# Optimization experiments

Measured on AMD Instinct MI355X. Metric: run time of the kernel, lower is better.

The kernel has to match this reference:

```python
import jax, jax.numpy as jnp
import numpy as np

EPS = 1e-5

def inorm(x):
    # instance norm over time (last) axis; torch.std is unbiased (ddof=1)
    m = jnp.mean(x, axis=-1, keepdims=True)
    s = jnp.sqrt(jnp.var(x, axis=-1, ddof=1, keepdims=True))
    return (x - m) / (s + EPS)

def tinorm(x):
    # time-wise instance norm: normalize over channel axis (dim=1)
    m = jnp.mean(x, axis=1, keepdims=True)
    s = jnp.sqrt(jnp.var(x, axis=1, ddof=1, keepdims=True))
    return (x - m) / (s + EPS)

def adaptive_norm(src, trg, wq, wk, wv, norm_fn):
    # src, trg: [B,C,T]; wq/wk/wv: [out,in] as in nn.Linear
    temp = src.shape[1] ** 0.5
    q = jnp.einsum('bct,oc->bto', norm_fn(src), wq)        # [B,Ts,C]
    k = jnp.einsum('bct,oc->bto', norm_fn(trg), wk)        # [B,Tt,C]
    v = jnp.einsum('bct,oc->bto', trg, wv)                 # [B,Tt,C]
    attn = jax.nn.softmax(jnp.einsum('bsc,btc->bst', q / temp, k), axis=-1)
    mean = jnp.einsum('bst,btc->bsc', attn, v)             # attn-weighted mean
    var = jax.nn.relu(jnp.einsum('bst,btc->bsc', attn, v * v) - mean * mean)
    mean_c = jnp.mean(mean, axis=1)[:, :, None]            # [B,C,1]
    std_c = jnp.sqrt(jnp.mean(var, axis=1))[:, :, None]    # [B,C,1]
    return std_c * inorm(src) + mean_c

def sap(x, w, b):
    # self-attention pooling over axis 1; x: [B,N,C], w: [C], b: [1]
    a = jax.nn.softmax(jnp.einsum('bnc,c->bn', x, w) + b, axis=-1)
    return jnp.einsum('bnc,bn->bc', x, a)

def setup_inputs():
    key = jax.random.key(0)
    ks = jax.random.split(key, 24)
    B, C, Ts, Tt, S = 4, 512, 2048, 2048, 2048
    sc = 1.0 / np.sqrt(C).astype(np.float32)
    return {
        'src': jax.random.normal(ks[0], (B, C, Ts), jnp.float32),
        'trg': jax.random.normal(ks[1], (B, C, Tt), jnp.float32),
        'means': jax.random.normal(ks[2], (B, S, C), jnp.float32),
        'stds': jax.random.uniform(ks[3], (B, S, C), jnp.float32),
        'wq_t': jax.random.normal(ks[4], (C, C), jnp.float32) * sc,
        'wk_t': jax.random.normal(ks[5], (C, C), jnp.float32) * sc,
        'wv_t': jax.random.normal(ks[6], (C, C), jnp.float32) * sc,
        'wq_c': jax.random.normal(ks[7], (C, C), jnp.float32) * sc,
        'wk_c': jax.random.normal(ks[8], (C, C), jnp.float32) * sc,
        'wv_c': jax.random.normal(ks[9], (C, C), jnp.float32) * sc,
        'conv1_w': jax.random.normal(ks[10], (C, 2 * C), jnp.float32) * sc,
        'conv1_b': jax.random.normal(ks[11], (C,), jnp.float32) * 0.02,
        'conv2_w': jax.random.normal(ks[12], (C, C, 3), jnp.float32) * sc,
        'bn_g': jax.random.uniform(ks[13], (C,), jnp.float32, 0.5, 1.5),
        'bn_b': jax.random.normal(ks[14], (C,), jnp.float32) * 0.05,
        'bn_m': jax.random.normal(ks[15], (C,), jnp.float32) * 0.1,
        'bn_v': jax.random.uniform(ks[16], (C,), jnp.float32, 0.5, 1.5),
        'msap_w': jax.random.normal(ks[17], (C,), jnp.float32) * sc,
        'msap_b': jax.random.normal(ks[18], (1,), jnp.float32) * 0.02,
        'ssap_w': jax.random.normal(ks[19], (C,), jnp.float32) * sc,
        'ssap_b': jax.random.normal(ks[20], (1,), jnp.float32) * 0.02,
    }

def reference(src, trg, means, stds, wq_t, wk_t, wv_t, wq_c, wk_c, wv_c,
              conv1_w, conv1_b, conv2_w, bn_g, bn_b, bn_m, bn_v,
              msap_w, msap_b, ssap_w, ssap_b):
    src1 = adaptive_norm(src, trg, wq_t, wk_t, wv_t, tinorm)   # TAN
    src2 = adaptive_norm(src, trg, wq_c, wk_c, wv_c, inorm)    # CAN
    x = jnp.concatenate([src1, src2], axis=1)                  # [B,2C,T]
    # conv1: kernel_size=1 -> pointwise GEMM
    x = jnp.einsum('bct,oc->bot', x, conv1_w) + conv1_b[None, :, None]
    # conv2: Conv1d(k=3, pad=1, bias=False) + BatchNorm1d(eval) + ReLU
    x = jax.lax.conv_general_dilated(x, conv2_w, (1,), 'SAME',
                                     dimension_numbers=('NCH', 'OIH', 'NCH'))
    x = (x - bn_m[None, :, None]) * jax.lax.rsqrt(bn_v[None, :, None] + EPS)
    x = x * bn_g[None, :, None] + bn_b[None, :, None]
    x = jax.nn.relu(x)
    # GLAN
    mean = sap(means, msap_w, msap_b)[:, :, None]              # [B,C,1]
    std = sap(stds, ssap_w, ssap_b)[:, :, None]                # [B,C,1]
    return inorm(x) * std + mean
```

## Files before the change

### kernel.cpp

```cpp
#include <hip/hip_runtime.h>
#include <cstdint>
#include <cstddef>

#define B_ 4
#define C_ 512
#define T_ 2048
#define S_ 2048
#define EPSF 1e-5f

typedef __bf16 bf16;
typedef __attribute__((ext_vector_type(8))) __bf16 bf16x8;
typedef __attribute__((ext_vector_type(4))) float f32x4;

__device__ __forceinline__ bf16 f2b(float f){ return (bf16)f; }
__device__ __forceinline__ float b2f(bf16 h){ return (float)h; }

__device__ __forceinline__ void gl_lds16(const void* g, void* l){
  __builtin_amdgcn_global_load_lds((__attribute__((address_space(1))) void*)(g),
                                   (__attribute__((address_space(3))) void*)(l), 16, 0, 0);
}

__device__ __forceinline__ float wave_sum(float v){
#pragma unroll
  for (int o = 32; o; o >>= 1) v += __shfl_xor(v, o, 64);
  return v;
}
__device__ __forceinline__ float wave_max(float v){
#pragma unroll
  for (int o = 32; o; o >>= 1) v = fmaxf(v, __shfl_xor(v, o, 64));
  return v;
}

template<int EPI, int TNW>
__global__ void __launch_bounds__(256) gemm_nt(
    const bf16* __restrict__ A, const bf16* __restrict__ Bm, void* __restrict__ Cout,
    int K, int lda, int ldb, int ldc,
    long long sA, long long sB, long long sC, long long sCb,
    int zdivA, int zmodB, float scale,
    const float* __restrict__ rs, const float* __restrict__ rsh,
    const float* __restrict__ cbias,
    float* __restrict__ osum, float* __restrict__ osum2, long long sRs,
    float* __restrict__ ocol)
{
  constexpr int TN = TNW*32;
  __shared__ alignas(16) bf16 lA[128*64];
  __shared__ alignas(16) bf16 lB[TN*64];
  __shared__ float redcs[EPI == 3 ? 32*68 : 1];
  const int tid = threadIdx.x;
  const int z = blockIdx.z;
  const bf16* Ab = A + (long long)(z / zdivA) * sA;
  const bf16* Bb = Bm + (long long)(z % zmodB) * sB;
  const int m0 = blockIdx.y*128, n0 = blockIdx.x*TN;
  const int lane = tid & 63, wvi = tid >> 6;
  const int wm = wvi >> 1, wn = wvi & 1;

  f32x4 acc[4][TNW] = {};

  const int lrow = tid >> 3;
  const int lcol = ((tid ^ lrow) & 7) * 8;
  const bf16* pa = Ab + (long long)(m0 + lrow)*lda + lcol;
  const bf16* pb = Bb + (long long)(n0 + lrow)*ldb + lcol;
  char* sa = (char*)lA + tid*16;
  char* sb = (char*)lB + tid*16;

  const int csg = tid >> 3, csph = tid & 7;
  float linv4[4];
  if (EPI == 3) {
#pragma unroll
    for (int rr = 0; rr < 4; ++rr)
      linv4[rr] = 1.f / rs[(long long)z*sRs + (m0 + csg*4 + rr)];
  }

  for (int k0 = 0; k0 < K; k0 += 64) {
#pragma unroll
    for (int it = 0; it < 4; ++it)
      gl_lds16(pa + (long long)it*32*lda + k0, sa + it*4096);
#pragma unroll
    for (int it = 0; it < TNW; ++it)
      gl_lds16(pb + (long long)it*32*ldb + k0, sb + it*4096);
    __syncthreads();
#pragma unroll
    for (int ks = 0; ks < 2; ++ks) {
      const int kq = ks*4 + (lane >> 4);
      bf16x8 af[4], bfr[TNW];
#pragma unroll
      for (int mt = 0; mt < 4; ++mt) {
        int r = wm*64 + mt*16 + (lane & 15);
        af[mt] = *(const bf16x8*)&lA[r*64 + ((kq ^ (r & 7))*8)];
      }
#pragma unroll
      for (int nt = 0; nt < TNW; ++nt) {
        int r = wn*(TNW*16) + nt*16 + (lane & 15);
        bfr[nt] = *(const bf16x8*)&lB[r*64 + ((kq ^ (r & 7))*8)];
      }
#pragma unroll
      for (int mt = 0; mt < 4; ++mt)
#pragma unroll
        for (int nt = 0; nt < TNW; ++nt)
          acc[mt][nt] = __builtin_amdgcn_mfma_f32_16x16x32_bf16(af[mt], bfr[nt], acc[mt][nt], 0, 0, 0);
    }
    bool own = false;
    if (EPI == 3) {
      own = ((k0 >> 6) & 3) == (int)blockIdx.x;
      if (own) {
        float part[8] = {0.f,0.f,0.f,0.f,0.f,0.f,0.f,0.f};
#pragma unroll
        for (int rr = 0; rr < 4; ++rr) {
          const int r = csg*4 + rr;
          bf16x8 v = *(const bf16x8*)&lA[r*64 + ((csph ^ (r & 7))*8)];
          const float li = linv4[rr];
#pragma unroll
          for (int j = 0; j < 8; ++j) part[j] += b2f(v[j]) * li;
        }
#pragma unroll
        for (int j = 0; j < 8; ++j) redcs[csg*68 + csph*8 + j] = part[j];
      }
    }
    __syncthreads();
    if (EPI == 3) {
      if (own && tid < 64) {
        float s = 0.f;
#pragma unroll
        for (int g2 = 0; g2 < 32; ++g2) s += redcs[g2*68 + tid];
        atomicAdd(&ocol[(long long)z*lda + k0 + tid], s);
      }
    }
  }

  if (EPI == 3) {
    float* red1 = (float*)lA;
    float* red2 = red1 + 4*TNW*16;
    const int cr = (lane >> 4)*4;
    float linv[4][4];
#pragma unroll
    for (int mt = 0; mt < 4; ++mt)
#pragma unroll
      for (int i = 0; i < 4; ++i)
        linv[mt][i] = 1.f / rs[(long long)z*sRs + (m0 + wm*64 + mt*16 + cr + i)];
    float s1[TNW], s2[TNW];
#pragma unroll
    for (int nt = 0; nt < TNW; ++nt) {
      s1[nt] = 0.f; s2[nt] = 0.f;
#pragma unroll
      for (int mt = 0; mt < 4; ++mt)
#pragma unroll
        for (int i = 0; i < 4; ++i) {
          float v = acc[mt][nt][i] * linv[mt][i];
          s1[nt] += v; s2[nt] += v*v;
        }
      s1[nt] += __shfl_xor(s1[nt], 16, 64);
      s1[nt] += __shfl_xor(s1[nt], 32, 64);
      s2[nt] += __shfl_xor(s2[nt], 16, 64);
      s2[nt] += __shfl_xor(s2[nt], 32, 64);
    }
    __syncthreads();
    if (lane < 16) {
#pragma unroll
      for (int nt = 0; nt < TNW; ++nt) {
        red1[(wvi*TNW + nt)*16 + lane] = s1[nt];
        red2[(wvi*TNW + nt)*16 + lane] = s2[nt];
      }
    }
    __syncthreads();
    if (tid < 2*TN) {
      const int which = tid >= TN;
      const int col = tid - which*TN;
      const int wn2 = col / (TNW*16), rem = col % (TNW*16);
      const float* rr = which ? red2 : red1;
      float v = rr[wn2*(TNW*16) + rem] + rr[(2+wn2)*(TNW*16) + rem];
      float* dst = which ? osum2 : osum;
      atomicAdd(&dst[sCb*z + n0 + col], v);
    }
    return;
  }

  const int cr = (lane >> 4)*4, cc = lane & 15;
#pragma unroll
  for (int mt = 0; mt < 4; ++mt) {
#pragma unroll
    for (int i = 0; i < 4; ++i) {
      const int mm = m0 + wm*64 + mt*16 + cr + i;
      float rsum = 0.f, rsum2 = 0.f;
#pragma unroll
      for (int nt = 0; nt < TNW; ++nt) {
        const int nn = n0 + wn*(TNW*16) + nt*16 + cc;
        float v = acc[mt][nt][i];
        const long long co = sC*z + (long long)mm*ldc + nn;
        if (EPI == 0) {
          v *= scale;
          if (cbias) v += cbias[sCb*z + nn];
          ((bf16*)Cout)[co] = f2b(v);
        } else if (EPI == 2) {
          v = fmaxf(v*rs[mm] + rsh[mm], 0.f);
          ((float*)Cout)[co] = v;
          rsum += v; rsum2 += v*v;
        } else if (EPI == 4) {
          v = __expf(v);
          ((bf16*)Cout)[co] = f2b(v);
          rsum += v;
        } else if (EPI == 5) {
          v = v*rs[(long long)z*sRs + mm] + rsh[(long long)z*sRs + mm]*cbias[sCb*z + nn];
          ((bf16*)Cout)[co] = f2b(v);
        }
      }
      if (EPI == 2 || EPI == 4) {
        rsum += __shfl_xor(rsum, 1, 64); rsum += __shfl_xor(rsum, 2, 64);
        rsum += __shfl_xor(rsum, 4, 64); rsum += __shfl_xor(rsum, 8, 64);
        if (EPI == 2) {
          rsum2 += __shfl_xor(rsum2, 1, 64); rsum2 += __shfl_xor(rsum2, 2, 64);
          rsum2 += __shfl_xor(rsum2, 4, 64); rsum2 += __shfl_xor(rsum2, 8, 64);
        }
        if (cc == 0) {
          atomicAdd(&osum[(long long)z*sRs + mm], rsum);
          if (EPI == 2) atomicAdd(&osum2[(long long)z*sRs + mm], rsum2);
        }
      }
    }
  }
}

__global__ void __launch_bounds__(512, 2) qk_exp_k(
    const bf16* __restrict__ QK, bf16* __restrict__ P, float* __restrict__ lsum)
{
  __shared__ alignas(16) char lds[135168];
  const int tid = threadIdx.x;
  const int bid = blockIdx.x;
  const int xcd = bid & 7, slot = bid >> 3;
  const int z  = (xcd >> 1) + ((slot >> 5) << 2);
  const int t  = (slot & 31) + ((xcd & 1) << 5);
  const int by = t >> 3, bx = t & 7;
  const int ph = z >> 2, b = z & 3;
  const bf16* Qb = QK + (long long)(b*2 + ph) * (2048LL*512);
  const bf16* Kb = QK + (long long)(8 + b*2 + ph) * (2048LL*512);
  const int m0 = by * 256, n0 = bx * 256;
  const int lane = tid & 63, wvi = tid >> 6;
  const int wm = wvi >> 2, wn = wvi & 3;
  const int l15 = lane & 15, lq = lane >> 4;
  const int swz = l15 & 7;

  f32x4 acc[8][4] = {};

  const int lr = tid >> 3;
  const int lc = ((tid ^ lr) & 7) * 8;
  const bf16* pa = Qb + (long long)(m0 + lr)*512 + lc;
  const bf16* pb = Kb + (long long)(n0 + lr)*512 + lc;

  auto STAGE = [&](int bb, int kt) {
    char* da = (char*)lds + bb*65536 + tid*16;
    const bf16* ga = pa + kt*64;
    const bf16* gb = pb + kt*64;
#pragma unroll
    for (int it = 0; it < 4; ++it) gl_lds16(ga + it*64*512, da + it*8192);
#pragma unroll
    for (int it = 0; it < 4; ++it) gl_lds16(gb + it*64*512, da + 32768 + it*8192);
  };

  STAGE(0, 0);
  for (int kt = 0; kt < 8; ++kt) {
    const int cur = kt & 1;
    if (kt < 7) {
      STAGE(cur ^ 1, kt + 1);
      asm volatile("s_waitcnt vmcnt(8)" ::: "memory");
    } else {
      asm volatile("s_waitcnt vmcnt(0)" ::: "memory");
    }
    __builtin_amdgcn_s_barrier();

    const bf16* lA = (const bf16*)(lds + cur*65536);
    const bf16* lB = lA + 16384;

    bf16x8 af[4], bfr[4];
#pragma unroll
    for (int half = 0; half < 4; ++half) {
      const int ks = half >> 1, mg = (half & 1) * 4;
      const int kq = ks*4 + lq;
      const int ko = (kq ^ swz) * 8;
      if ((half & 1) == 0) {
#pragma unroll
        for (int nt = 0; nt < 4; ++nt)
          bfr[nt] = *(const bf16x8*)&lB[(wn*64 + nt*16 + l15)*64 + ko];
      }
#pragma unroll
      for (int mt = 0; mt < 4; ++mt)
        af[mt] = *(const bf16x8*)&lA[(wm*128 + (mg + mt)*16 + l15)*64 + ko];
      __builtin_amdgcn_s_barrier();
      __builtin_amdgcn_s_setprio(1);
#pragma unroll
      for (int mt = 0; mt < 4; ++mt)
#pragma unroll
        for (int nt = 0; nt < 4; ++nt)
          acc[mg + mt][nt] = __builtin_amdgcn_mfma_f32_16x16x32_bf16(
              af[mt], bfr[nt], acc[mg + mt][nt], 0, 0, 0);
      __builtin_amdgcn_s_setprio(0);
      __builtin_amdgcn_s_barrier();
    }
  }

  constexpr int LDC = 264;
  bf16* lC = (bf16*)lds;
  const long long zT = (long long)z * 2048;
  float* lrw = lsum + zT;
  const int cr = lq * 4;
#pragma unroll
  for (int mt = 0; mt < 8; ++mt) {
#pragma unroll
    for (int i = 0; i < 4; ++i) {
      const int mmL = wm*128 + mt*16 + cr + i;
      float rsum = 0.f;
#pragma unroll
      for (int nt = 0; nt < 4; ++nt) {
        const int nnL = wn*64 + nt*16 + l15;
        float v = __expf(acc[mt][nt][i]);
        lC[mmL*LDC + nnL] = f2b(v);
        rsum += v;
      }
      rsum += __shfl_xor(rsum, 1, 64); rsum += __shfl_xor(rsum, 2, 64);
      rsum += __shfl_xor(rsum, 4, 64); rsum += __shfl_xor(rsum, 8, 64);
      if (l15 == 0) atomicAdd(&lrw[m0 + mmL], rsum);
    }
  }
  __syncthreads();
  bf16* Cb = P + zT * 2048;
#pragma unroll
  for (int j = 0; j < 16; ++j) {
    const int flat = j*512 + tid;
    const int r = flat >> 5, c16 = flat & 31;
    const f32x4 v = *(const f32x4*)&lC[r*LDC + c16*8];
    *(f32x4*)&Cb[(long long)(m0 + r)*2048 + n0 + c16*8] = v;
  }
}

__global__ void __launch_bounds__(256) row_stats_k(const float* __restrict__ X1,
    const float* __restrict__ X2, float* __restrict__ Mo, float* __restrict__ So, int n1)
{
  __shared__ float r1[4], r2[4];
  const int row = blockIdx.x;
  const float* x = (row < n1) ? X1 + (long long)row*T_ : X2 + (long long)(row-n1)*T_;
  float s1 = 0.f, s2 = 0.f;
  for (int i = threadIdx.x; i < T_; i += 256){ float v = x[i]; s1 += v; s2 += v*v; }
  s1 = wave_sum(s1); s2 = wave_sum(s2);
  const int lane = threadIdx.x & 63, w = threadIdx.x >> 6;
  if (!lane){ r1[w] = s1; r2[w] = s2; }
  __syncthreads();
  if (threadIdx.x == 0){
    s1 = r1[0]+r1[1]+r1[2]+r1[3];
    s2 = r2[0]+r2[1]+r2[2]+r2[3];
    float m = s1 * (1.f/T_);
    float var = (s2 - s1*m) * (1.f/(T_-1));
    Mo[row] = m; So[row] = sqrtf(fmaxf(var, 0.f));
  }
}

__global__ void __launch_bounds__(256) col_stats_k(const float* __restrict__ src,
    const float* __restrict__ trg, float* __restrict__ Mo, float* __restrict__ So)
{
  __shared__ float r1[4][64], r2[4][64];
  const int z = blockIdx.y, t0 = blockIdx.x*64;
  const float* X = (z < B_) ? src : trg;
  const int b = z & (B_-1);
  const int tl = threadIdx.x & 63, cg = threadIdx.x >> 6;
  float s1 = 0.f, s2 = 0.f;
  for (int c = cg; c < C_; c += 4) {
    float v = X[((long long)b*C_ + c)*T_ + t0 + tl];
    s1 += v; s2 += v*v;
  }
  r1[cg][tl] = s1; r2[cg][tl] = s2;
  __syncthreads();
  if (cg == 0) {
    s1 = r1[0][tl]+r1[1][tl]+r1[2][tl]+r1[3][tl];
    s2 = r2[0][tl]+r2[1][tl]+r2[2][tl]+r2[3][tl];
    float m = s1 * (1.f/C_);
    float var = (s2 - s1*m) * (1.f/(C_-1));
    Mo[z*T_ + t0 + tl] = m;
    So[z*T_ + t0 + tl] = sqrtf(fmaxf(var, 0.f));
  }
}

__global__ void __launch_bounds__(256) transform_k(const float* __restrict__ src,
    const float* __restrict__ trg, bf16* __restrict__ XT)
{
  __shared__ float tile[32][33];
  const int z = blockIdx.z, t0 = blockIdx.x*32, c0 = blockIdx.y*32;
  const int is_t = z >= B_, b = z & (B_-1);
  const float* X = is_t ? trg : src;
  const int tx = threadIdx.x, ty = threadIdx.y;
#pragma unroll
  for (int r = 0; r < 4; ++r) {
    int ci = ty + r*8;
    tile[ci][tx] = X[((long long)b*C_ + c0 + ci)*T_ + t0 + tx];
  }
  __syncthreads();
#pragma unroll
  for (int r = 0; r < 4; ++r) {
    int tj = ty + r*8, ci = tx;
    XT[((long long)z*T_ + t0 + tj)*C_ + c0 + ci] = f2b(tile[ci][tj]);
  }
}

__global__ void __launch_bounds__(256) foldqk_k(
    const float* __restrict__ wq_c, const float* __restrict__ wq_t,
    const float* __restrict__ wk_c, const float* __restrict__ wk_t,
    const float* __restrict__ inm, const float* __restrict__ ins,
    bf16* __restrict__ W, float* __restrict__ cb)
{
  __shared__ float r1[4];
  const int o = blockIdx.x, z = blockIdx.y;
  const int side = z >> 3, b = (z >> 1) & 3, ph = z & 1;
  const float* w = side ? (ph ? wk_t : wk_c) : (ph ? wq_t : wq_c);
  const float sc = side ? 1.f : 0.044194173824159216f;
  const int ofs = (side*B_ + b)*C_;
  float acc = 0.f;
  for (int c = threadIdx.x; c < C_; c += 256) {
    float wv = w[o*C_ + c] * sc;
    float out, contrib;
    if (ph == 0) {
      float ri = 1.f / (ins[ofs + c] + EPSF);
      out = wv * ri;
      contrib = -out * inm[ofs + c];
    } else {
      out = wv;
      contrib = wv;
    }
    W[((long long)z*C_ + o)*C_ + c] = f2b(out);
    acc += contrib;
  }
  acc = wave_sum(acc);
  const int lane = threadIdx.x & 63, wq = threadIdx.x >> 6;
  if (!lane) r1[wq] = acc;
  __syncthreads();
  if (threadIdx.x == 0) cb[z*C_ + o] = r1[0]+r1[1]+r1[2]+r1[3];
}

__global__ void __launch_bounds__(256) rsfill_k(
    const float* __restrict__ tnm, const float* __restrict__ tns,
    float* __restrict__ rsq, float* __restrict__ rshq)
{
  const int z = blockIdx.y, t = blockIdx.x*256 + threadIdx.x;
  const int side = z >> 3, b = (z >> 1) & 3, ph = z & 1;
  float rv, rh;
  if (ph == 0) { rv = 1.f; rh = 1.f; }
  else {
    const int ofs = (side*B_ + b)*T_;
    float r = 1.f / (tns[ofs + t] + EPSF);
    rv = r; rh = -tnm[ofs + t] * r;
  }
  rsq[z*T_ + t] = rv; rshq[z*T_ + t] = rh;
}

__global__ void __launch_bounds__(256) softmax_row_k(const float* __restrict__ X, float* __restrict__ O)
{
  __shared__ float red[4];
  const long long row = blockIdx.x;
  const float* x = X + row*T_ + threadIdx.x*8;
  float v[8];
  f32x4 a0 = *(const f32x4*)x;
  f32x4 a1 = *(const f32x4*)(x + 4);
#pragma unroll
  for (int j = 0; j < 4; ++j){ v[j] = a0[j]; v[4+j] = a1[j]; }
  float m = -3.4e38f;
#pragma unroll
  for (int j = 0; j < 8; ++j) m = fmaxf(m, v[j]);
  m = wave_max(m);
  const int lane = threadIdx.x & 63, w = threadIdx.x >> 6;
  if (!lane) red[w] = m;
  __syncthreads();
  m = fmaxf(fmaxf(red[0], red[1]), fmaxf(red[2], red[3]));
  __syncthreads();
  float s = 0.f;
#pragma unroll
  for (int j = 0; j < 8; ++j){ v[j] = __expf(v[j] - m); s += v[j]; }
  s = wave_sum(s);
  if (!lane) red[w] = s;
  __syncthreads();
  s = red[0]+red[1]+red[2]+red[3];
  const float inv = 1.f/s;
  float* o = O + row*T_ + threadIdx.x*8;
#pragma unroll
  for (int j = 0; j < 8; ++j) o[j] = v[j]*inv;
}

__global__ void __launch_bounds__(256) vv_fin_k(const float* __restrict__ cs,
    const bf16* __restrict__ VT, const float* __restrict__ msum,
    const float* __restrict__ m2sum, float* __restrict__ meanc, float* __restrict__ stdc)
{
  __shared__ float r1[4];
  const int c = blockIdx.x, z = blockIdx.y;
  const bf16* vr = VT + ((long long)z*C_ + c)*T_;
  const float* w = cs + z*T_;
  float a = 0.f;
  for (int t = threadIdx.x; t < T_; t += 256){ float v = b2f(vr[t]); a += w[t]*v*v; }
  a = wave_sum(a);
  const int lane = threadIdx.x & 63, wq = threadIdx.x >> 6;
  if (!lane) r1[wq] = a;
  __syncthreads();
  if (threadIdx.x == 0){
    a = r1[0]+r1[1]+r1[2]+r1[3];
    const int idx = z*C_ + c;
    meanc[idx] = msum[idx] * (1.f/S_);
    float var = (a - m2sum[idx]) * (1.f/S_);
    stdc[idx] = sqrtf(fmaxf(var, 0.f));
  }
}

__global__ void __launch_bounds__(256) weff_k(const float* __restrict__ w1,
    const float* __restrict__ b1, const float* __restrict__ sdt, const float* __restrict__ sdc,
    const float* __restrict__ mct, const float* __restrict__ mcc,
    const float* __restrict__ inm, const float* __restrict__ ins,
    bf16* __restrict__ Weff, float* __restrict__ beff)
{
  __shared__ float r1[4];
  const int o = blockIdx.x, b = blockIdx.y;
  const int ofs = b*C_;
  float accb = 0.f;
  for (int c = threadIdx.x; c < C_; c += 256) {
    float wa = w1[o*2*C_ + c], wb = w1[o*2*C_ + C_ + c];
    float s = wa*sdt[b*C_+c] + wb*sdc[b*C_+c];
    float w2 = s / (ins[ofs + c] + EPSF);
    Weff[((long long)(b*C_ + o))*C_ + c] = f2b(w2);
    accb += wa*mct[b*C_+c] + wb*mcc[b*C_+c] - w2*inm[ofs + c];
  }
  accb = wave_sum(accb);
  const int lane = threadIdx.x & 63, w = threadIdx.x >> 6;
  if (!lane) r1[w] = accb;
  __syncthreads();
  if (threadIdx.x == 0) beff[b*C_ + o] = b1[o] + r1[0]+r1[1]+r1[2]+r1[3];
}

__global__ void __launch_bounds__(256) w2r_k(const float* __restrict__ w2,
    const float* __restrict__ g, const float* __restrict__ be,
    const float* __restrict__ mu, const float* __restrict__ va,
    bf16* __restrict__ W2r, float* __restrict__ bnsc, float* __restrict__ bnsh)
{
  const int o = blockIdx.x;
  for (int c = threadIdx.x; c < C_; c += 256)
#pragma unroll
    for (int dt = 0; dt < 3; ++dt)
      W2r[(long long)o*3*C_ + dt*C_ + c] = f2b(w2[((long long)o*C_ + c)*3 + dt]);
  if (threadIdx.x == 0) {
    float s = g[o] * rsqrtf(va[o] + EPSF);
    bnsc[o] = s;
    bnsh[o] = be[o] - mu[o]*s;
  }
}

__global__ void __launch_bounds__(256) castv_k(const float* __restrict__ a0,
    const float* __restrict__ a1, bf16* __restrict__ o)
{
  const int i = blockIdx.x*256 + threadIdx.x;
  o[i] = f2b(((i >> 18) ? a1 : a0)[i & 262143]);
}

__global__ void __launch_bounds__(256) zero_pad_k(bf16* __restrict__ x1p)
{
  const int i = blockIdx.x*256 + threadIdx.x;
  const int b = i >> 10, rem = i & 1023;
  const long long row = (rem >> 9) ? (T_+1) : 0;
  const int c = rem & (C_-1);
  x1p[((long long)b*(T_+2) + row)*C_ + c] = f2b(0.f);
}

__global__ void __launch_bounds__(256) zero_f32_k(float* __restrict__ p)
{
  p[blockIdx.x*256 + threadIdx.x] = 0.f;
}

__global__ void __launch_bounds__(256) sap_logit_k(const float* __restrict__ means,
    const float* __restrict__ stds, const float* __restrict__ mw, const float* __restrict__ sw,
    const float* __restrict__ mb, const float* __restrict__ sb, float* __restrict__ out)
{
  const int n = blockIdx.x*4 + (threadIdx.x >> 6);
  const int z = blockIdx.y;
  const int sel = z >= B_, b = z & (B_-1);
  const float* x = sel ? stds : means;
  const float* w = sel ? sw : mw;
  const int lane = threadIdx.x & 63;
  const float* p = x + ((long long)b*S_ + n)*C_;
  float a = 0.f;
  for (int c = lane; c < C_; c += 64) a += p[c]*w[c];
  a = wave_sum(a);
  if (!lane) out[z*S_ + n] = a + (sel ? sb[0] : mb[0]);
}

__global__ void __launch_bounds__(256) sap_wsum_k(const float* __restrict__ means,
    const float* __restrict__ stds, const float* __restrict__ a, float* __restrict__ out)
{
  const int c = blockIdx.x*256 + threadIdx.x;
  const int z = blockIdx.z;
  const int sel = z >= B_, b = z & (B_-1);
  const float* x = sel ? stds : means;
  const long long n0 = (long long)blockIdx.y*256;
  const float* p = x + ((long long)b*S_ + n0)*C_ + c;
  const float* aw = a + z*S_ + n0;
  float acc = 0.f;
  for (int n = 0; n < 256; ++n) acc += p[(long long)n*C_] * aw[n];
  atomicAdd(&out[z*C_ + c], acc);
}

__global__ void __launch_bounds__(256) final_k(const float* __restrict__ y,
    const float* __restrict__ ysum, const float* __restrict__ y2sum,
    const float* __restrict__ sapms, float* __restrict__ out)
{
  const long long i = (long long)(blockIdx.x*256 + threadIdx.x) * 4;
  const long long r = i >> 11;
  const float s1 = ysum[r], s2 = y2sum[r];
  const float m = s1 * (1.f/T_);
  const float var = (s2 - s1*m) * (1.f/(T_-1));
  const float inv = 1.f/(sqrtf(fmaxf(var, 0.f)) + EPSF);
  const float mn = sapms[r], sd = sapms[B_*C_ + r];
  const f32x4 v = *(const f32x4*)(y + i);
  f32x4 o;
#pragma unroll
  for (int j = 0; j < 4; ++j) o[j] = (v[j] - m)*inv*sd + mn;
  *(f32x4*)(out + i) = o;
}

extern "C" void kernel_launch(void* const* d_in, const int* in_sizes, int n_in,
                              void* d_out, int out_size, void* d_ws, size_t ws_size,
                              hipStream_t stream)
{
  (void)in_sizes; (void)n_in; (void)out_size; (void)ws_size;
  const float* src    = (const float*)d_in[0];
  const float* trg    = (const float*)d_in[1];
  const float* means  = (const float*)d_in[2];
  const float* stds   = (const float*)d_in[3];
  const float* conv1w = (const float*)d_in[10];
  const float* conv1b = (const float*)d_in[11];
  const float* conv2w = (const float*)d_in[12];
  const float* bn_g   = (const float*)d_in[13];
  const float* bn_b   = (const float*)d_in[14];
  const float* bn_m   = (const float*)d_in[15];
  const float* bn_v   = (const float*)d_in[16];
  const float* msap_w = (const float*)d_in[17];
  const float* msap_b = (const float*)d_in[18];
  const float* ssap_w = (const float*)d_in[19];
  const float* ssap_b = (const float*)d_in[20];

  const long long BTC = (long long)B_*T_*C_;
  const long long TC  = (long long)T_*C_;

  char* p = (char*)d_ws;
  auto take = [&](size_t n)->char*{ char* r = p; p += (n + 255) & ~(size_t)255; return r; };

  bf16* P2  = (bf16*)take((size_t)2*B_*S_*T_*2);
  bf16* QK4 = (bf16*)take((size_t)16*TC*2);
  bf16* VT2 = (bf16*)take((size_t)2*BTC*2);
  bf16* WQeff = (bf16*)take((size_t)16*C_*C_*2);
  bf16* WVb = (bf16*)take((size_t)2*C_*C_*2);
  bf16* Weff= (bf16*)take((size_t)B_*C_*C_*2);
  bf16* W2r = (bf16*)take((size_t)C_*3*C_*2);
  bf16* x1p = (bf16*)take((size_t)B_*(T_+2)*C_*2);
  float* y  = (float*)take((size_t)B_*C_*T_*4);
  bf16* XT  = (bf16*)y;
  float* colsum = (float*)take(2*B_*T_*4);
  float* msum   = (float*)take(2*B_*C_*4);
  float* m2sum  = (float*)take(2*B_*C_*4);
  float* sapms  = (float*)take(2*B_*C_*4);
  float* lrow   = (float*)take(2*B_*S_*4);
  float* ysum   = (float*)take(B_*C_*4);
  float* y2sum  = (float*)take(B_*C_*4);
  float* tnm = (float*)take(2*B_*T_*4);
  float* tns = (float*)take(2*B_*T_*4);
  float* inm = (float*)take(2*B_*C_*4);
  float* ins = (float*)take(2*B_*C_*4);
  float* meanc = (float*)take(2*B_*C_*4);
  float* stdc  = (float*)take(2*B_*C_*4);
  float* beff  = (float*)take(B_*C_*4);
  float* bnsc  = (float*)take(C_*4);
  float* bnsh  = (float*)take(C_*4);
  float* sapl  = (float*)take(2*B_*S_*4);
  float* sapa  = (float*)take(2*B_*S_*4);
  float* cbq   = (float*)take(16*C_*4);
  float* rsq   = (float*)take(16*T_*4);
  float* rshq  = (float*)take(16*T_*4);

  dim3 blk(256);

  castv_k<<<2048, blk, 0, stream>>>((const float*)d_in[9], (const float*)d_in[6], WVb);
  w2r_k<<<C_, blk, 0, stream>>>(conv2w, bn_g, bn_b, bn_m, bn_v, W2r, bnsc, bnsh);
  row_stats_k<<<2*B_*C_, blk, 0, stream>>>(src, trg, inm, ins, B_*C_);
  col_stats_k<<<dim3(T_/64, 2*B_), blk, 0, stream>>>(src, trg, tnm, tns);
  transform_k<<<dim3(T_/32, C_/32, 2*B_), dim3(32,8), 0, stream>>>(src, trg, XT);
  foldqk_k<<<dim3(C_, 16), blk, 0, stream>>>((const float*)d_in[7], (const float*)d_in[4],
      (const float*)d_in[8], (const float*)d_in[5], inm, ins, WQeff, cbq);
  rsfill_k<<<dim3(T_/256, 16), blk, 0, stream>>>(tnm, tns, rsq, rshq);
  zero_pad_k<<<16, blk, 0, stream>>>(x1p);
  zero_f32_k<<<192, blk, 0, stream>>>(colsum);

  gemm_nt<5,4><<<dim3(C_/128, T_/128, 16), blk, 0, stream>>>(XT, WQeff, QK4,
      C_, C_, C_, C_, TC, (long long)C_*C_, TC, C_,
      2, 16, 1.f, rsq, rshq, cbq, nullptr, nullptr, T_, nullptr);
  gemm_nt<0,2><<<dim3(T_/64, C_/128, 8), blk, 0, stream>>>(WVb, XT + 4*TC, VT2,
      C_, C_, C_, T_, (long long)C_*C_, TC, (long long)C_*T_, 0, 4, 4, 1.f,
      nullptr, nullptr, nullptr, nullptr, nullptr, 0, nullptr);
  qk_exp_k<<<dim3(512), dim3(512), 0, stream>>>(QK4, P2, lrow);
  gemm_nt<3,4><<<dim3(C_/128, S_/128, 8), blk, 0, stream>>>(P2, VT2, nullptr,
      T_, T_, T_, 0, (long long)S_*T_, (long long)C_*T_, 0, C_, 1, 8, 1.f,
      lrow, nullptr, nullptr, msum, m2sum, S_, colsum);
  vv_fin_k<<<dim3(C_, 2*B_), blk, 0, stream>>>(colsum, VT2, msum, m2sum, meanc, stdc);

  weff_k<<<dim3(C_, B_), blk, 0, stream>>>(conv1w, conv1b,
      stdc + B_*C_, stdc, meanc + B_*C_, meanc, inm, ins, Weff, beff);
  gemm_nt<0,2><<<dim3(C_/64, T_/128, B_), blk, 0, stream>>>(XT, Weff, x1p + C_,
      C_, C_, C_, C_, TC, (long long)C_*C_, (long long)(T_+2)*C_, C_,
      1, 8, 1.f, nullptr, nullptr, beff, nullptr, nullptr, 0, nullptr);
  gemm_nt<2,2><<<dim3(T_/64, C_/128, B_), blk, 0, stream>>>(W2r, x1p, y,
      3*C_, 3*C_, C_, T_, 0, (long long)(T_+2)*C_, (long long)C_*T_, 0,
      1, 8, 1.f, bnsc, bnsh, nullptr, ysum, y2sum, C_, nullptr);

  sap_logit_k<<<dim3(S_/4, 2*B_), blk, 0, stream>>>(means, stds, msap_w, ssap_w,
      msap_b, ssap_b, sapl);
  softmax_row_k<<<2*B_, blk, 0, stream>>>(sapl, sapa);
  sap_wsum_k<<<dim3(C_/256, S_/256, 2*B_), blk, 0, stream>>>(means, stds, sapa, sapms);

  final_k<<<4096, blk, 0, stream>>>(y, ysum, y2sum, sapms, (float*)d_out);
}
```

Baseline: 452.9 us.

## Fuse row/column stats into transpose-cast kernel with atomic partial sums

Merges the row statistics, column statistics and bf16 transpose kernels into one pass that loads each src/trg tile once, writes the transposed bf16 data with packed 32-bit stores, and accumulates row and column sums via atomics. A small finalize kernel turns the sums into means and stds. The zeroing launch is widened so it also clears the new accumulators, assuming they sit right after colsum in the buffer. The intent is to read the two input tensors once instead of three times, at the cost of extra atomics and a different float summation order.

Result: faster. 420.5 us (-7.2%).

```diff
diff --git a/kernel.cpp b/kernel.cpp
--- a/kernel.cpp
+++ b/kernel.cpp
@@ -330,70 +330,83 @@
   }
 }
 
-__global__ void __launch_bounds__(256) row_stats_k(const float* __restrict__ X1,
-    const float* __restrict__ X2, float* __restrict__ Mo, float* __restrict__ So, int n1)
-{
-  __shared__ float r1[4], r2[4];
-  const int row = blockIdx.x;
-  const float* x = (row < n1) ? X1 + (long long)row*T_ : X2 + (long long)(row-n1)*T_;
-  float s1 = 0.f, s2 = 0.f;
-  for (int i = threadIdx.x; i < T_; i += 256){ float v = x[i]; s1 += v; s2 += v*v; }
-  s1 = wave_sum(s1); s2 = wave_sum(s2);
-  const int lane = threadIdx.x & 63, w = threadIdx.x >> 6;
-  if (!lane){ r1[w] = s1; r2[w] = s2; }
-  __syncthreads();
-  if (threadIdx.x == 0){
-    s1 = r1[0]+r1[1]+r1[2]+r1[3];
-    s2 = r2[0]+r2[1]+r2[2]+r2[3];
-    float m = s1 * (1.f/T_);
-    float var = (s2 - s1*m) * (1.f/(T_-1));
-    Mo[row] = m; So[row] = sqrtf(fmaxf(var, 0.f));
-  }
-}
-
-__global__ void __launch_bounds__(256) col_stats_k(const float* __restrict__ src,
-    const float* __restrict__ trg, float* __restrict__ Mo, float* __restrict__ So)
-{
-  __shared__ float r1[4][64], r2[4][64];
-  const int z = blockIdx.y, t0 = blockIdx.x*64;
-  const float* X = (z < B_) ? src : trg;
-  const int b = z & (B_-1);
-  const int tl = threadIdx.x & 63, cg = threadIdx.x >> 6;
-  float s1 = 0.f, s2 = 0.f;
-  for (int c = cg; c < C_; c += 4) {
-    float v = X[((long long)b*C_ + c)*T_ + t0 + tl];
-    s1 += v; s2 += v*v;
-  }
-  r1[cg][tl] = s1; r2[cg][tl] = s2;
-  __syncthreads();
-  if (cg == 0) {
-    s1 = r1[0][tl]+r1[1][tl]+r1[2][tl]+r1[3][tl];
-    s2 = r2[0][tl]+r2[1][tl]+r2[2][tl]+r2[3][tl];
-    float m = s1 * (1.f/C_);
-    float var = (s2 - s1*m) * (1.f/(C_-1));
-    Mo[z*T_ + t0 + tl] = m;
-    So[z*T_ + t0 + tl] = sqrtf(fmaxf(var, 0.f));
-  }
-}
-
-__global__ void __launch_bounds__(256) transform_k(const float* __restrict__ src,
-    const float* __restrict__ trg, bf16* __restrict__ XT)
-{
-  __shared__ float tile[32][33];
-  const int z = blockIdx.z, t0 = blockIdx.x*32, c0 = blockIdx.y*32;
+__global__ void __launch_bounds__(256) transform_stats_k(
+    const float* __restrict__ src, const float* __restrict__ trg,
+    bf16* __restrict__ XT, float* __restrict__ rsum, float* __restrict__ rsum2,
+    float* __restrict__ csum, float* __restrict__ csum2)
+{
+  __shared__ float tile[64][33];
+  __shared__ float rp1[64][4], rp2[64][4];
+  __shared__ float cp1[32][8], cp2[32][8];
+  const int z = blockIdx.z, t0 = blockIdx.x*32, c0 = blockIdx.y*64;
   const int is_t = z >= B_, b = z & (B_-1);
   const float* X = is_t ? trg : src;
-  const int tx = threadIdx.x, ty = threadIdx.y;
+  const int tid = threadIdx.x;
+  const int tx = tid & 31, cy = tid >> 5;
+#pragma unroll
+  for (int it = 0; it < 8; ++it) {
+    const int cl = cy + it*8;
+    tile[cl][tx] = X[((long long)b*C_ + c0 + cl)*T_ + t0 + tx];
+  }
+  __syncthreads();
+  const int l32 = tid & 31, tq = tid >> 5;
 #pragma unroll
   for (int r = 0; r < 4; ++r) {
-    int ci = ty + r*8;
-    tile[ci][tx] = X[((long long)b*C_ + c0 + ci)*T_ + t0 + tx];
-  }
-  __syncthreads();
-#pragma unroll
-  for (int r = 0; r < 4; ++r) {
-    int tj = ty + r*8, ci = tx;
-    XT[((long long)z*T_ + t0 + tj)*C_ + c0 + ci] = f2b(tile[ci][tj]);
+    const int tl = r*8 + tq;
+    bf16 b0 = f2b(tile[2*l32][tl]), b1 = f2b(tile[2*l32+1][tl]);
+    unsigned short u0, u1;
+    __builtin_memcpy(&u0, &b0, 2); __builtin_memcpy(&u1, &b1, 2);
+    const unsigned int pk = (unsigned int)u0 | ((unsigned int)u1 << 16);
+    *(unsigned int*)&XT[((long long)z*T_ + t0 + tl)*C_ + c0 + 2*l32] = pk;
+  }
+  {
+    const int cl = tid >> 2, g = tid & 3;
+    float s1 = 0.f, s2 = 0.f;
+#pragma unroll
+    for (int k = 0; k < 8; ++k){ float v = tile[cl][g + 4*k]; s1 += v; s2 += v*v; }
+    rp1[cl][g] = s1; rp2[cl][g] = s2;
+  }
+  {
+    const int tl = tid >> 3, g = tid & 7;
+    float s1 = 0.f, s2 = 0.f;
+#pragma unroll
+    for (int k = 0; k < 8; ++k){ float v = tile[g + 8*k][tl]; s1 += v; s2 += v*v; }
+    cp1[tl][g] = s1; cp2[tl][g] = s2;
+  }
+  __syncthreads();
+  if (tid < 64) {
+    float s1 = rp1[tid][0]+rp1[tid][1]+rp1[tid][2]+rp1[tid][3];
+    float s2 = rp2[tid][0]+rp2[tid][1]+rp2[tid][2]+rp2[tid][3];
+    atomicAdd(&rsum[z*C_ + c0 + tid], s1);
+    atomicAdd(&rsum2[z*C_ + c0 + tid], s2);
+  } else if (tid < 96) {
+    const int tl = tid - 64;
+    float s1 = 0.f, s2 = 0.f;
+#pragma unroll
+    for (int g = 0; g < 8; ++g){ s1 += cp1[tl][g]; s2 += cp2[tl][g]; }
+    atomicAdd(&csum[z*T_ + t0 + tl], s1);
+    atomicAdd(&csum2[z*T_ + t0 + tl], s2);
+  }
+}
+
+__global__ void __launch_bounds__(256) statfin_k(
+    const float* __restrict__ rsum, const float* __restrict__ rsum2,
+    const float* __restrict__ csum, const float* __restrict__ csum2,
+    float* __restrict__ inm, float* __restrict__ ins,
+    float* __restrict__ tnm, float* __restrict__ tns)
+{
+  const int i = blockIdx.x*256 + threadIdx.x;
+  if (i < 2*B_*C_) {
+    const float s1 = rsum[i], s2 = rsum2[i];
+    const float m = s1 * (1.f/T_);
+    const float var = (s2 - s1*m) * (1.f/(T_-1));
+    inm[i] = m; ins[i] = sqrtf(fmaxf(var, 0.f));
+  } else {
+    const int j = i - 2*B_*C_;
+    const float s1 = csum[j], s2 = csum2[j];
+    const float m = s1 * (1.f/C_);
+    const float var = (s2 - s1*m) * (1.f/(C_-1));
+    tnm[j] = m; tns[j] = sqrtf(fmaxf(var, 0.f));
   }
 }
 
@@ -658,6 +671,10 @@
   float* lrow   = (float*)take(2*B_*S_*4);
   float* ysum   = (float*)take(B_*C_*4);
   float* y2sum  = (float*)take(B_*C_*4);
+  float* rsum   = (float*)take(2*B_*C_*4);
+  float* rsum2  = (float*)take(2*B_*C_*4);
+  float* csum   = (float*)take(2*B_*T_*4);
+  float* csum2  = (float*)take(2*B_*T_*4);
   float* tnm = (float*)take(2*B_*T_*4);
   float* tns = (float*)take(2*B_*T_*4);
   float* inm = (float*)take(2*B_*C_*4);
@@ -675,16 +692,16 @@
 
   dim3 blk(256);
 
+  zero_f32_k<<<352, blk, 0, stream>>>(colsum);
   castv_k<<<2048, blk, 0, stream>>>((const float*)d_in[9], (const float*)d_in[6], WVb);
   w2r_k<<<C_, blk, 0, stream>>>(conv2w, bn_g, bn_b, bn_m, bn_v, W2r, bnsc, bnsh);
-  row_stats_k<<<2*B_*C_, blk, 0, stream>>>(src, trg, inm, ins, B_*C_);
-  col_stats_k<<<dim3(T_/64, 2*B_), blk, 0, stream>>>(src, trg, tnm, tns);
-  transform_k<<<dim3(T_/32, C_/32, 2*B_), dim3(32,8), 0, stream>>>(src, trg, XT);
+  transform_stats_k<<<dim3(T_/32, C_/64, 2*B_), blk, 0, stream>>>(src, trg, XT,
+      rsum, rsum2, csum, csum2);
+  statfin_k<<<80, blk, 0, stream>>>(rsum, rsum2, csum, csum2, inm, ins, tnm, tns);
   foldqk_k<<<dim3(C_, 16), blk, 0, stream>>>((const float*)d_in[7], (const float*)d_in[4],
       (const float*)d_in[8], (const float*)d_in[5], inm, ins, WQeff, cbq);
   rsfill_k<<<dim3(T_/256, 16), blk, 0, stream>>>(tnm, tns, rsq, rshq);
   zero_pad_k<<<16, blk, 0, stream>>>(x1p);
-  zero_f32_k<<<192, blk, 0, stream>>>(colsum);
 
   gemm_nt<5,4><<<dim3(C_/128, T_/128, 16), blk, 0, stream>>>(XT, WQeff, QK4,
       C_, C_, C_, C_, TC, (long long)C_*C_, TC, C_,
```
